# Performance work log

Measured on AMD Instinct MI355X. Metric: run time of the kernel, lower is better.

## Reference

```python
import jax, jax.numpy as jnp
import numpy as np

DIM = 128
N_HEADS = 16
HEAD_DIM = DIM // N_HEADS  # 8
HIDDEN = 344  # multiple_of=8 rounding of int(2*4*128/3)
B, S = 4, 2048


def setup_inputs() -> dict:
    key = jax.random.key(0)
    ks = jax.random.split(key, 8)
    sc = 0.05
    return {
        "x": jax.random.normal(ks[0], (B, S, DIM), dtype=jnp.float32),
        "wq": jax.random.normal(ks[1], (DIM, DIM), dtype=jnp.float32) * sc,
        "wk": jax.random.normal(ks[2], (DIM, DIM), dtype=jnp.float32) * sc,
        "wv": jax.random.normal(ks[3], (DIM, DIM), dtype=jnp.float32) * sc,
        "wo": jax.random.normal(ks[4], (DIM, DIM), dtype=jnp.float32) * sc,
        "w1": jax.random.normal(ks[5], (DIM, HIDDEN), dtype=jnp.float32) * sc,
        "w3": jax.random.normal(ks[6], (DIM, HIDDEN), dtype=jnp.float32) * sc,
        "w2": jax.random.normal(ks[7], (HIDDEN, DIM), dtype=jnp.float32) * sc,
    }


def reference(x, wq, wk, wv, wo, w1, w3, w2):
    bsz, seqlen, _ = x.shape
    # --- Attention (no scaling, no mask, per source) ---
    q = (x @ wq).reshape(bsz, seqlen, N_HEADS, HEAD_DIM)
    k = (x @ wk).reshape(bsz, seqlen, N_HEADS, HEAD_DIM)
    v = (x @ wv).reshape(bsz, seqlen, N_HEADS, HEAD_DIM)
    # scores: [B, H, S, S]
    scores = jnp.einsum("bqhd,bkhd->bhqk", q, k)
    probs = jax.nn.softmax(scores.astype(jnp.float32), axis=-1).astype(q.dtype)
    attn = jnp.einsum("bhqk,bkhd->bqhd", probs, v).reshape(bsz, seqlen, DIM)
    h = x + attn @ wo
    # --- SwiGLU FFN ---
    ffn = (jax.nn.silu(h @ w1) * (h @ w3)) @ w2
    return h + ffn
```

## Files before the change

kernel.cpp:

```cpp
#include <hip/hip_runtime.h>
#include <hip/hip_bf16.h>
#include <stdint.h>
#include <math.h>

typedef __attribute__((ext_vector_type(8))) short short8;
typedef __attribute__((ext_vector_type(4))) float f32x4;

#define NTHREADS 256
#define DIM 128
#define NH 16
#define HD 8
#define HIDDEN 344
#define HIDP 352
#define BATCH 4
#define SEQ 2048
#define MROWS (BATCH * SEQ)
#define LOG2E 1.4426950408889634f

static __device__ __forceinline__ uint16_t f2bf(float f) {
  union { float f; uint32_t u; } v; v.f = f;
  uint32_t r = v.u + 0x7FFFu + ((v.u >> 16) & 1u);
  return (uint16_t)(r >> 16);
}
static __device__ __forceinline__ uint32_t pk2(float lo, float hi) {
  union { __hip_bfloat162 b; uint32_t u; } c;
  c.b = __float22bfloat162_rn(make_float2(lo, hi));
  return c.u;
}
#define MAGIC_BF 12599163.0f
static __device__ __forceinline__ uint32_t pke2(float a, float b) {
  const float ua = fmaf(a, 128.0f, MAGIC_BF);
  const float ub = fmaf(b, 128.0f, MAGIC_BF);
  return __builtin_amdgcn_perm(__builtin_bit_cast(uint32_t, ub),
                               __builtin_bit_cast(uint32_t, ua), 0x05040100u);
}
static __device__ __forceinline__ f32x4 mfma32(short8 a, short8 b, f32x4 c) {
  return __builtin_amdgcn_mfma_f32_16x16x32_bf16(a, b, c, 0, 0, 0);
}

__global__ __launch_bounds__(256) void prep_kernel(
    const float* __restrict__ wq,
    const float* __restrict__ wk, const float* __restrict__ wv,
    const float* __restrict__ wo, const float* __restrict__ w1,
    const float* __restrict__ w3, const float* __restrict__ w2,
    uint16_t* __restrict__ qkv_t,
    uint16_t* __restrict__ wo_t,  uint16_t* __restrict__ w1_t,
    uint16_t* __restrict__ w3_t,  uint16_t* __restrict__ w2_t)
{
  const int nt  = gridDim.x * blockDim.x;
  const int tid = blockIdx.x * blockDim.x + threadIdx.x;
  for (int i = tid; i < 384 * 128; i += nt) {
    int n = i >> 7, k = i & 127;
    const float* w = (n < 128) ? wq : ((n < 256) ? wk : wv);
    const float s = (n < 128) ? LOG2E : 1.0f;
    qkv_t[i] = f2bf(w[k * 128 + (n & 127)] * s);
  }
  for (int i = tid; i < 128 * 128; i += nt) {
    int n = i >> 7, k = i & 127;
    wo_t[i] = f2bf(wo[k * 128 + n]);
  }
  for (int i = tid; i < 384 * 128; i += nt) {
    int n = i >> 7, k = i & 127;
    w1_t[i] = (n < HIDDEN) ? f2bf(w1[k * HIDDEN + n]) : (uint16_t)0;
    w3_t[i] = (n < HIDDEN) ? f2bf(w3[k * HIDDEN + n]) : (uint16_t)0;
  }
  for (int i = tid; i < 128 * HIDP; i += nt) {
    int n = i / HIDP, k = i - n * HIDP;
    w2_t[i] = (k < HIDDEN) ? f2bf(w2[k * 128 + n]) : (uint16_t)0;
  }
}

__global__ __launch_bounds__(256, 4) void qkv_gemm(
    const float* __restrict__ Av, const uint16_t* __restrict__ B1t,
    uint16_t* __restrict__ outb,
    uint16_t* __restrict__ kc_o, uint16_t* __restrict__ vt_o)
{
  const int tid = threadIdx.x;
  const int w = tid >> 6, l = tid & 63;
  const int lg = l >> 4, lm = l & 15;
  const int row0 = blockIdx.x * 64 + w * 16;
  const int col0 = blockIdx.y * 64;

  const uint16_t* Bp = B1t + (size_t)(col0 + lm) * 128 + lg * 8;
  short8 bA0 = *(const short8*)(Bp);
  short8 bA1 = *(const short8*)(Bp + 32);
  short8 bA2 = *(const short8*)(Bp + 64);
  short8 bA3 = *(const short8*)(Bp + 96);

  short8 af[4];
  const float* Af = Av + (size_t)(row0 + lm) * 128 + lg * 8;
#pragma unroll
  for (int ks = 0; ks < 4; ++ks) {
    const f32x4 a0 = *(const f32x4*)(Af + ks * 32);
    const f32x4 a1 = *(const f32x4*)(Af + ks * 32 + 4);
    union { uint32_t u[4]; short8 s8; } cv;
    cv.u[0] = pk2(a0[0], a0[1]); cv.u[1] = pk2(a0[2], a0[3]);
    cv.u[2] = pk2(a1[0], a1[1]); cv.u[3] = pk2(a1[2], a1[3]);
    af[ks] = cv.s8;
  }

  f32x4 acc[4];
#pragma unroll
  for (int t = 0; t < 4; ++t) acc[t] = (f32x4){0.f, 0.f, 0.f, 0.f};

  short8 bB0 = *(const short8*)(Bp + 2048);
  short8 bB1 = *(const short8*)(Bp + 2048 + 32);
  short8 bB2 = *(const short8*)(Bp + 2048 + 64);
  short8 bB3 = *(const short8*)(Bp + 2048 + 96);
  acc[0] = mfma32(af[0], bA0, acc[0]);
  acc[0] = mfma32(af[1], bA1, acc[0]);
  acc[0] = mfma32(af[2], bA2, acc[0]);
  acc[0] = mfma32(af[3], bA3, acc[0]);
  bA0 = *(const short8*)(Bp + 4096);
  bA1 = *(const short8*)(Bp + 4096 + 32);
  bA2 = *(const short8*)(Bp + 4096 + 64);
  bA3 = *(const short8*)(Bp + 4096 + 96);
  acc[1] = mfma32(af[0], bB0, acc[1]);
  acc[1] = mfma32(af[1], bB1, acc[1]);
  acc[1] = mfma32(af[2], bB2, acc[1]);
  acc[1] = mfma32(af[3], bB3, acc[1]);
  bB0 = *(const short8*)(Bp + 6144);
  bB1 = *(const short8*)(Bp + 6144 + 32);
  bB2 = *(const short8*)(Bp + 6144 + 64);
  bB3 = *(const short8*)(Bp + 6144 + 96);
  acc[2] = mfma32(af[0], bA0, acc[2]);
  acc[2] = mfma32(af[1], bA1, acc[2]);
  acc[2] = mfma32(af[2], bA2, acc[2]);
  acc[2] = mfma32(af[3], bA3, acc[2]);
  acc[3] = mfma32(af[0], bB0, acc[3]);
  acc[3] = mfma32(af[1], bB1, acc[3]);
  acc[3] = mfma32(af[2], bB2, acc[3]);
  acc[3] = mfma32(af[3], bB3, acc[3]);

#pragma unroll
  for (int t = 0; t < 4; ++t) {
#pragma unroll
    for (int r = 0; r < 4; ++r) {
      const int row = row0 + lg * 4 + r;
      const int col = col0 + t * 16 + lm;
      const float v = acc[t][r];
      const int bb = row >> 11, ss = row & 2047;
      if (col < 128) {
        outb[(size_t)row * 128 + col] = f2bf(v);
      } else if (col < 256) {
        const int c = col - 128;
        kc_o[((size_t)((bb << 4) + (c >> 3)) * SEQ + ss) * 8 + (c & 7)] = f2bf(v);
      } else {
        const int c = col - 256;
        vt_o[((size_t)(bb * 128 + c)) * SEQ + ss] = f2bf(v);
      }
    }
  }
}

__global__ __launch_bounds__(256, 4) void attn_kernel(
    const uint16_t* __restrict__ qb,
    const uint16_t* __restrict__ kc,
    const uint16_t* __restrict__ vt,
    uint16_t* __restrict__ attn_o)
{
  __shared__ __attribute__((aligned(16))) float part[4][64][32];

  const int tid = threadIdx.x;
  const int w = tid >> 6, l = tid & 63;
  const int lg = l >> 4, lm = l & 15;
  int bid = blockIdx.x;
  bid = (bid & 7) * 128 + (bid >> 3);
  const int qc = bid & 15;
  const int bh = bid >> 4;
  const int b = bh >> 4, h = bh & 15;
  const int q0 = qc * 128;
  const int kh = w;

  const short8 zero8 = {0, 0, 0, 0, 0, 0, 0, 0};
  const f32x4 zero4 = {0.f, 0.f, 0.f, 0.f};
  const short ob = (short)0x3F80;
  const short8 ones8 = {ob, ob, ob, ob, ob, ob, ob, ob};

  short8 qf[8];
#pragma unroll
  for (int t = 0; t < 8; ++t) {
    qf[t] = zero8;
    if (lg == 0)
      qf[t] = *(const short8*)(qb + (size_t)(b * SEQ + q0 + t * 16 + lm) * DIM + h * HD);
  }

  const uint16_t* kp = kc + (size_t)bh * SEQ * HD +
                       (kh * 512 + 8 * (lm >> 2) + (lm & 3)) * HD;
  const uint16_t* vp = vt + (size_t)(bh * HD + (lm & 7)) * SEQ + kh * 512 + lg * 8;

  short8 k0 = zero8, k1 = zero8, k2 = zero8, k3 = zero8;
  short8 v0 = (lm == 8) ? ones8 : zero8;
  short8 v1 = v0;

  f32x4 acc[8];
#pragma unroll
  for (int t = 0; t < 8; ++t) acc[t] = zero4;

#define LK()                                       \
  do { if (lg == 0) {                              \
    k0 = *(const short8*)(kp);                     \
    k1 = *(const short8*)(kp + 32);                \
    k2 = *(const short8*)(kp + 256);               \
    k3 = *(const short8*)(kp + 288); }             \
    kp += 512; } while (0)

#define LV()                                       \
  do { if (lm < HD) {                              \
    v0 = *(const short8*)(vp);                     \
    v1 = *(const short8*)(vp + 32); }              \
    vp += 64; } while (0)

#define PACKP(SA, SB, OUT)                 \
  do { union { uint32_t u[4]; short8 s; } _t; \
    _t.u[0] = pke2(SA[0], SA[1]);          \
    _t.u[1] = pke2(SA[2], SA[3]);          \
    _t.u[2] = pke2(SB[0], SB[1]);          \
    _t.u[3] = pke2(SB[2], SB[3]);          \
    OUT = _t.s; } while (0)

  LK();
  LV();

#pragma unroll 1
  for (int it = 0; it < 8; ++it) {
#pragma unroll
    for (int t = 0; t < 8; ++t) {
      f32x4 s0 = mfma32(k0, qf[t], zero4);
      f32x4 s1 = mfma32(k1, qf[t], zero4);
      f32x4 s2 = mfma32(k2, qf[t], zero4);
      f32x4 s3 = mfma32(k3, qf[t], zero4);
      if (t == 7) LK();
      short8 p0, p1;
      PACKP(s0, s1, p0);
      PACKP(s2, s3, p1);
      acc[t] = mfma32(v0, p0, acc[t]);
      acc[t] = mfma32(v1, p1, acc[t]);
      if (t == 7) LV();
    }
  }

#undef LK
#undef LV
#undef PACKP

#pragma unroll
  for (int t = 0; t < 8; ++t) *(f32x4*)&part[w][l][t * 4] = acc[t];
  __syncthreads();

#pragma unroll
  for (int j = 0; j < 2; ++j) {
    const int tt = w * 2 + j;
    const f32x4 m = (*(const f32x4*)&part[0][l][tt * 4] +
                     *(const f32x4*)&part[1][l][tt * 4]) +
                    (*(const f32x4*)&part[2][l][tt * 4] +
                     *(const f32x4*)&part[3][l][tt * 4]);
    const float inv = 1.0f / __shfl(m[0], 32 + lm);
    if (lg < 2) {
      const size_t o = (size_t)(b * SEQ + q0 + tt * 16 + lm) * DIM + h * HD + lg * 4;
      *(uint32_t*)(attn_o + o)     = pk2(m[0] * inv, m[1] * inv);
      *(uint32_t*)(attn_o + o + 2) = pk2(m[2] * inv, m[3] * inv);
    }
  }
}

__global__ __launch_bounds__(512, 4) void ffn_kernel(
    const uint16_t* __restrict__ attn_o,
    const float* __restrict__ x,
    const uint16_t* __restrict__ wo_t,
    const uint16_t* __restrict__ w1_t,
    const uint16_t* __restrict__ w3_t,
    const uint16_t* __restrict__ w2_t,
    float* __restrict__ out)
{
  __shared__ __attribute__((aligned(16))) uint16_t h_l[16][136];
  __shared__ __attribute__((aligned(16))) uint16_t u_l[16][360];

  const int tid = threadIdx.x;
  const int w = tid >> 6, l = tid & 63;
  const int lg = l >> 4, lm = l & 15;
  const int R0 = blockIdx.x * 16;

  short8 af[4], wof[4], b1a[4], b3a[4];
  {
    const uint16_t* Ap = attn_o + (size_t)(R0 + lm) * 128 + lg * 8;
    const uint16_t* Bp = wo_t + (size_t)(w * 16 + lm) * 128 + lg * 8;
    const uint16_t* B1p = w1_t + (size_t)(w * 16 + lm) * 128 + lg * 8;
    const uint16_t* B3p = w3_t + (size_t)(w * 16 + lm) * 128 + lg * 8;
#pragma unroll
    for (int ks = 0; ks < 4; ++ks) {
      af[ks]  = *(const short8*)(Ap + ks * 32);
      wof[ks] = *(const short8*)(Bp + ks * 32);
      b1a[ks] = *(const short8*)(B1p + ks * 32);
      b3a[ks] = *(const short8*)(B3p + ks * 32);
    }
  }

  float hreg[4];
  {
    f32x4 a0 = (f32x4){0.f, 0.f, 0.f, 0.f};
    f32x4 a1 = (f32x4){0.f, 0.f, 0.f, 0.f};
    a0 = mfma32(af[0], wof[0], a0);
    a1 = mfma32(af[1], wof[1], a1);
    a0 = mfma32(af[2], wof[2], a0);
    a1 = mfma32(af[3], wof[3], a1);
    const f32x4 acc = a0 + a1;
#pragma unroll
    for (int r = 0; r < 4; ++r) {
      const float h = acc[r] + x[(size_t)(R0 + lg * 4 + r) * 128 + w * 16 + lm];
      hreg[r] = h;
      h_l[lg * 4 + r][w * 16 + lm] = f2bf(h);
    }
  }
  __syncthreads();

  short8 af2[4];
#pragma unroll
  for (int ks = 0; ks < 4; ++ks)
    af2[ks] = *(const short8*)&h_l[lm][ks * 32 + lg * 8];

  {
    f32x4 ag = (f32x4){0.f, 0.f, 0.f, 0.f};
    f32x4 ae = (f32x4){0.f, 0.f, 0.f, 0.f};
#pragma unroll
    for (int ks = 0; ks < 4; ++ks) {
      ag = mfma32(af2[ks], b1a[ks], ag);
      ae = mfma32(af2[ks], b3a[ks], ae);
    }
    const int ct2 = w + 8;
    const uint16_t* B1p = w1_t + (size_t)(ct2 * 16 + lm) * 128 + lg * 8;
    const uint16_t* B3p = w3_t + (size_t)(ct2 * 16 + lm) * 128 + lg * 8;
#pragma unroll
    for (int ks = 0; ks < 4; ++ks) {
      b1a[ks] = *(const short8*)(B1p + ks * 32);
      b3a[ks] = *(const short8*)(B3p + ks * 32);
    }
#pragma unroll
    for (int r = 0; r < 4; ++r) {
      const float g = ag[r];
      const float u = g / (1.f + __expf(-g)) * ae[r];
      u_l[lg * 4 + r][w * 16 + lm] = f2bf(u);
    }
  }
  {
    const int ct = w + 8;
    f32x4 ag = (f32x4){0.f, 0.f, 0.f, 0.f};
    f32x4 ae = (f32x4){0.f, 0.f, 0.f, 0.f};
#pragma unroll
    for (int ks = 0; ks < 4; ++ks) {
      ag = mfma32(af2[ks], b1a[ks], ag);
      ae = mfma32(af2[ks], b3a[ks], ae);
    }
    if (w < 6) {
      const int ct3 = w + 16;
      const uint16_t* B1p = w1_t + (size_t)(ct3 * 16 + lm) * 128 + lg * 8;
      const uint16_t* B3p = w3_t + (size_t)(ct3 * 16 + lm) * 128 + lg * 8;
#pragma unroll
      for (int ks = 0; ks < 4; ++ks) {
        b1a[ks] = *(const short8*)(B1p + ks * 32);
        b3a[ks] = *(const short8*)(B3p + ks * 32);
      }
    }
#pragma unroll
    for (int r = 0; r < 4; ++r) {
      const float g = ag[r];
      const float u = g / (1.f + __expf(-g)) * ae[r];
      u_l[lg * 4 + r][ct * 16 + lm] = f2bf(u);
    }
  }
  if (w < 6) {
    const int ct = w + 16;
    f32x4 ag = (f32x4){0.f, 0.f, 0.f, 0.f};
    f32x4 ae = (f32x4){0.f, 0.f, 0.f, 0.f};
#pragma unroll
    for (int ks = 0; ks < 4; ++ks) {
      ag = mfma32(af2[ks], b1a[ks], ag);
      ae = mfma32(af2[ks], b3a[ks], ae);
    }
#pragma unroll
    for (int r = 0; r < 4; ++r) {
      const float g = ag[r];
      const float u = g / (1.f + __expf(-g)) * ae[r];
      u_l[lg * 4 + r][ct * 16 + lm] = f2bf(u);
    }
  }
  __syncthreads();

  {
    short8 w2f0, w2f1, w2f2, w2f3;
    const uint16_t* Bp = w2_t + (size_t)(w * 16 + lm) * HIDP + lg * 8;
    w2f0 = *(const short8*)(Bp);
    w2f1 = *(const short8*)(Bp + 32);
    w2f2 = *(const short8*)(Bp + 64);
    w2f3 = *(const short8*)(Bp + 96);
    f32x4 acce = (f32x4){0.f, 0.f, 0.f, 0.f};
    f32x4 acco = (f32x4){0.f, 0.f, 0.f, 0.f};
    acce = mfma32(*(const short8*)&u_l[lm][0 * 32 + lg * 8], w2f0, acce);
    w2f0 = *(const short8*)(Bp + 128);
    acco = mfma32(*(const short8*)&u_l[lm][1 * 32 + lg * 8], w2f1, acco);
    w2f1 = *(const short8*)(Bp + 160);
    acce = mfma32(*(const short8*)&u_l[lm][2 * 32 + lg * 8], w2f2, acce);
    w2f2 = *(const short8*)(Bp + 192);
    acco = mfma32(*(const short8*)&u_l[lm][3 * 32 + lg * 8], w2f3, acco);
    w2f3 = *(const short8*)(Bp + 224);
    acce = mfma32(*(const short8*)&u_l[lm][4 * 32 + lg * 8], w2f0, acce);
    w2f0 = *(const short8*)(Bp + 256);
    acco = mfma32(*(const short8*)&u_l[lm][5 * 32 + lg * 8], w2f1, acco);
    w2f1 = *(const short8*)(Bp + 288);
    acce = mfma32(*(const short8*)&u_l[lm][6 * 32 + lg * 8], w2f2, acce);
    w2f2 = *(const short8*)(Bp + 320);
    acco = mfma32(*(const short8*)&u_l[lm][7 * 32 + lg * 8], w2f3, acco);
    acce = mfma32(*(const short8*)&u_l[lm][8 * 32 + lg * 8], w2f0, acce);
    acco = mfma32(*(const short8*)&u_l[lm][9 * 32 + lg * 8], w2f1, acco);
    acce = mfma32(*(const short8*)&u_l[lm][10 * 32 + lg * 8], w2f2, acce);
    const f32x4 acc = acce + acco;
#pragma unroll
    for (int r = 0; r < 4; ++r)
      out[(size_t)(R0 + lg * 4 + r) * 128 + w * 16 + lm] = hreg[r] + acc[r];
  }
}

extern "C" void kernel_launch(void* const* d_in, const int* in_sizes, int n_in,
                              void* d_out, int out_size, void* d_ws, size_t ws_size,
                              hipStream_t stream) {
  const float* x  = (const float*)d_in[0];
  const float* wq = (const float*)d_in[1];
  const float* wk = (const float*)d_in[2];
  const float* wv = (const float*)d_in[3];
  const float* wo = (const float*)d_in[4];
  const float* w1 = (const float*)d_in[5];
  const float* w3 = (const float*)d_in[6];
  const float* w2 = (const float*)d_in[7];
  float* out = (float*)d_out;

  char* ws = (char*)d_ws;
  size_t off = 0;
  auto alloc = [&](size_t bytes) {
    size_t o = off;
    off += (bytes + 255) & ~(size_t)255;
    return o;
  };
  uint16_t* qkv_t  = (uint16_t*)(ws + alloc(384 * 128 * 2));
  uint16_t* wo_t   = (uint16_t*)(ws + alloc(128 * 128 * 2));
  uint16_t* w1_t   = (uint16_t*)(ws + alloc(384 * 128 * 2));
  uint16_t* w3_t   = (uint16_t*)(ws + alloc(384 * 128 * 2));
  uint16_t* w2_t   = (uint16_t*)(ws + alloc(128 * HIDP * 2));
  uint16_t* q_buf  = (uint16_t*)(ws + alloc((size_t)MROWS * DIM * 2));
  uint16_t* kc_b   = (uint16_t*)(ws + alloc((size_t)MROWS * DIM * 2));
  uint16_t* vt_b   = (uint16_t*)(ws + alloc((size_t)MROWS * DIM * 2));
  uint16_t* attn_o = (uint16_t*)(ws + alloc((size_t)MROWS * DIM * 2));

  prep_kernel<<<512, 256, 0, stream>>>(wq, wk, wv, wo, w1, w3, w2,
                                       qkv_t, wo_t, w1_t, w3_t, w2_t);
  qkv_gemm<<<dim3(MROWS / 64, 6), 256, 0, stream>>>(
      x, qkv_t, q_buf, kc_b, vt_b);
  attn_kernel<<<dim3(BATCH * NH * (SEQ / 128)), 256, 0, stream>>>(
      q_buf, kc_b, vt_b, attn_o);
  ffn_kernel<<<dim3(MROWS / 16), 512, 0, stream>>>(
      attn_o, x, wo_t, w1_t, w3_t, w2_t, out);
}
```

Baseline: 63.52 us.

## Process 32 rows per FFN block to reuse weight fragments across two row tiles

The FFN kernel now handles two 16-row tiles per block, so each loaded wo/w1/w3/w2 weight fragment feeds two MFMAs instead of one. This halves the per-row weight fragment traffic from L2 and doubles the independent MFMA chains. The grid is halved, and register and LDS use per block grow, so the launch bound drops to 2 blocks per CU, which reduces occupancy.

```diff
diff --git a/kernel.cpp b/kernel.cpp
--- a/kernel.cpp
+++ b/kernel.cpp
@@ -264,7 +264,7 @@
   }
 }
 
-__global__ __launch_bounds__(512, 4) void ffn_kernel(
+__global__ __launch_bounds__(512, 2) void ffn_kernel(
     const uint16_t* __restrict__ attn_o,
     const float* __restrict__ x,
     const uint16_t* __restrict__ wo_t,
@@ -273,117 +273,104 @@
     const uint16_t* __restrict__ w2_t,
     float* __restrict__ out)
 {
-  __shared__ __attribute__((aligned(16))) uint16_t h_l[16][136];
-  __shared__ __attribute__((aligned(16))) uint16_t u_l[16][360];
+  __shared__ __attribute__((aligned(16))) uint16_t h_l[2][16][136];
+  __shared__ __attribute__((aligned(16))) uint16_t u_l[2][16][360];
 
   const int tid = threadIdx.x;
   const int w = tid >> 6, l = tid & 63;
   const int lg = l >> 4, lm = l & 15;
-  const int R0 = blockIdx.x * 16;
-
-  short8 af[4], wof[4], b1a[4], b3a[4];
+  const int R0 = blockIdx.x * 32;
+
+  short8 af0[4], af1[4], wof[4], b1a[4], b3a[4];
   {
-    const uint16_t* Ap = attn_o + (size_t)(R0 + lm) * 128 + lg * 8;
+    const uint16_t* Ap0 = attn_o + (size_t)(R0 + lm) * 128 + lg * 8;
+    const uint16_t* Ap1 = attn_o + (size_t)(R0 + 16 + lm) * 128 + lg * 8;
     const uint16_t* Bp = wo_t + (size_t)(w * 16 + lm) * 128 + lg * 8;
     const uint16_t* B1p = w1_t + (size_t)(w * 16 + lm) * 128 + lg * 8;
     const uint16_t* B3p = w3_t + (size_t)(w * 16 + lm) * 128 + lg * 8;
 #pragma unroll
     for (int ks = 0; ks < 4; ++ks) {
-      af[ks]  = *(const short8*)(Ap + ks * 32);
+      af0[ks] = *(const short8*)(Ap0 + ks * 32);
+      af1[ks] = *(const short8*)(Ap1 + ks * 32);
       wof[ks] = *(const short8*)(Bp + ks * 32);
       b1a[ks] = *(const short8*)(B1p + ks * 32);
       b3a[ks] = *(const short8*)(B3p + ks * 32);
     }
   }
 
-  float hreg[4];
+  float h0reg[4], h1reg[4];
   {
-    f32x4 a0 = (f32x4){0.f, 0.f, 0.f, 0.f};
-    f32x4 a1 = (f32x4){0.f, 0.f, 0.f, 0.f};
-    a0 = mfma32(af[0], wof[0], a0);
-    a1 = mfma32(af[1], wof[1], a1);
-    a0 = mfma32(af[2], wof[2], a0);
-    a1 = mfma32(af[3], wof[3], a1);
-    const f32x4 acc = a0 + a1;
+    f32x4 p00 = (f32x4){0.f, 0.f, 0.f, 0.f};
+    f32x4 p01 = (f32x4){0.f, 0.f, 0.f, 0.f};
+    f32x4 p10 = (f32x4){0.f, 0.f, 0.f, 0.f};
+    f32x4 p11 = (f32x4){0.f, 0.f, 0.f, 0.f};
+    p00 = mfma32(af0[0], wof[0], p00);
+    p10 = mfma32(af1[0], wof[0], p10);
+    p01 = mfma32(af0[1], wof[1], p01);
+    p11 = mfma32(af1[1], wof[1], p11);
+    p00 = mfma32(af0[2], wof[2], p00);
+    p10 = mfma32(af1[2], wof[2], p10);
+    p01 = mfma32(af0[3], wof[3], p01);
+    p11 = mfma32(af1[3], wof[3], p11);
+    const f32x4 a0 = p00 + p01;
+    const f32x4 a1 = p10 + p11;
 #pragma unroll
     for (int r = 0; r < 4; ++r) {
-      const float h = acc[r] + x[(size_t)(R0 + lg * 4 + r) * 128 + w * 16 + lm];
-      hreg[r] = h;
-      h_l[lg * 4 + r][w * 16 + lm] = f2bf(h);
+      const float h0 = a0[r] + x[(size_t)(R0 + lg * 4 + r) * 128 + w * 16 + lm];
+      const float h1 = a1[r] + x[(size_t)(R0 + 16 + lg * 4 + r) * 128 + w * 16 + lm];
+      h0reg[r] = h0;
+      h1reg[r] = h1;
+      h_l[0][lg * 4 + r][w * 16 + lm] = f2bf(h0);
+      h_l[1][lg * 4 + r][w * 16 + lm] = f2bf(h1);
     }
   }
   __syncthreads();
 
-  short8 af2[4];
-#pragma unroll
-  for (int ks = 0; ks < 4; ++ks)
-    af2[ks] = *(const short8*)&h_l[lm][ks * 32 + lg * 8];
-
-  {
-    f32x4 ag = (f32x4){0.f, 0.f, 0.f, 0.f};
-    f32x4 ae = (f32x4){0.f, 0.f, 0.f, 0.f};
-#pragma unroll
-    for (int ks = 0; ks < 4; ++ks) {
-      ag = mfma32(af2[ks], b1a[ks], ag);
-      ae = mfma32(af2[ks], b3a[ks], ae);
-    }
-    const int ct2 = w + 8;
-    const uint16_t* B1p = w1_t + (size_t)(ct2 * 16 + lm) * 128 + lg * 8;
-    const uint16_t* B3p = w3_t + (size_t)(ct2 * 16 + lm) * 128 + lg * 8;
-#pragma unroll
-    for (int ks = 0; ks < 4; ++ks) {
-      b1a[ks] = *(const short8*)(B1p + ks * 32);
-      b3a[ks] = *(const short8*)(B3p + ks * 32);
-    }
-#pragma unroll
-    for (int r = 0; r < 4; ++r) {
-      const float g = ag[r];
-      const float u = g / (1.f + __expf(-g)) * ae[r];
-      u_l[lg * 4 + r][w * 16 + lm] = f2bf(u);
-    }
-  }
-  {
-    const int ct = w + 8;
-    f32x4 ag = (f32x4){0.f, 0.f, 0.f, 0.f};
-    f32x4 ae = (f32x4){0.f, 0.f, 0.f, 0.f};
-#pragma unroll
-    for (int ks = 0; ks < 4; ++ks) {
-      ag = mfma32(af2[ks], b1a[ks], ag);
-      ae = mfma32(af2[ks], b3a[ks], ae);
-    }
-    if (w < 6) {
-      const int ct3 = w + 16;
-      const uint16_t* B1p = w1_t + (size_t)(ct3 * 16 + lm) * 128 + lg * 8;
-      const uint16_t* B3p = w3_t + (size_t)(ct3 * 16 + lm) * 128 + lg * 8;
-#pragma unroll
-      for (int ks = 0; ks < 4; ++ks) {
-        b1a[ks] = *(const short8*)(B1p + ks * 32);
-        b3a[ks] = *(const short8*)(B3p + ks * 32);
-      }
-    }
-#pragma unroll
-    for (int r = 0; r < 4; ++r) {
-      const float g = ag[r];
-      const float u = g / (1.f + __expf(-g)) * ae[r];
-      u_l[lg * 4 + r][ct * 16 + lm] = f2bf(u);
-    }
-  }
-  if (w < 6) {
-    const int ct = w + 16;
-    f32x4 ag = (f32x4){0.f, 0.f, 0.f, 0.f};
-    f32x4 ae = (f32x4){0.f, 0.f, 0.f, 0.f};
-#pragma unroll
-    for (int ks = 0; ks < 4; ++ks) {
-      ag = mfma32(af2[ks], b1a[ks], ag);
-      ae = mfma32(af2[ks], b3a[ks], ae);
-    }
-#pragma unroll
-    for (int r = 0; r < 4; ++r) {
-      const float g = ag[r];
-      const float u = g / (1.f + __expf(-g)) * ae[r];
-      u_l[lg * 4 + r][ct * 16 + lm] = f2bf(u);
-    }
-  }
+  short8 afh0[4], afh1[4];
+#pragma unroll
+  for (int ks = 0; ks < 4; ++ks) {
+    afh0[ks] = *(const short8*)&h_l[0][lm][ks * 32 + lg * 8];
+    afh1[ks] = *(const short8*)&h_l[1][lm][ks * 32 + lg * 8];
+  }
+
+#define BSTAGE(CT, PREFETCH_CT, DO_PREFETCH)                        \
+  do {                                                              \
+    f32x4 g0 = (f32x4){0.f, 0.f, 0.f, 0.f};                         \
+    f32x4 e0 = (f32x4){0.f, 0.f, 0.f, 0.f};                         \
+    f32x4 g1 = (f32x4){0.f, 0.f, 0.f, 0.f};                         \
+    f32x4 e1 = (f32x4){0.f, 0.f, 0.f, 0.f};                         \
+    _Pragma("unroll")                                               \
+    for (int ks = 0; ks < 4; ++ks) {                                \
+      g0 = mfma32(afh0[ks], b1a[ks], g0);                           \
+      g1 = mfma32(afh1[ks], b1a[ks], g1);                           \
+      e0 = mfma32(afh0[ks], b3a[ks], e0);                           \
+      e1 = mfma32(afh1[ks], b3a[ks], e1);                           \
+    }                                                               \
+    if (DO_PREFETCH) {                                              \
+      const uint16_t* B1p = w1_t + (size_t)((PREFETCH_CT) * 16 + lm) * 128 + lg * 8; \
+      const uint16_t* B3p = w3_t + (size_t)((PREFETCH_CT) * 16 + lm) * 128 + lg * 8; \
+      _Pragma("unroll")                                             \
+      for (int ks = 0; ks < 4; ++ks) {                              \
+        b1a[ks] = *(const short8*)(B1p + ks * 32);                  \
+        b3a[ks] = *(const short8*)(B3p + ks * 32);                  \
+      }                                                             \
+    }                                                               \
+    _Pragma("unroll")                                               \
+    for (int r = 0; r < 4; ++r) {                                   \
+      const float ga = g0[r];                                       \
+      const float gb = g1[r];                                       \
+      const float u0 = ga / (1.f + __expf(-ga)) * e0[r];            \
+      const float u1 = gb / (1.f + __expf(-gb)) * e1[r];            \
+      u_l[0][lg * 4 + r][(CT) * 16 + lm] = f2bf(u0);                \
+      u_l[1][lg * 4 + r][(CT) * 16 + lm] = f2bf(u1);                \
+    }                                                               \
+  } while (0)
+
+  BSTAGE(w, w + 8, 1);
+  BSTAGE(w + 8, w + 16, (w < 6));
+  if (w < 6) BSTAGE(w + 16, 0, 0);
+
+#undef BSTAGE
   __syncthreads();
 
   {
@@ -393,30 +380,33 @@
     w2f1 = *(const short8*)(Bp + 32);
     w2f2 = *(const short8*)(Bp + 64);
     w2f3 = *(const short8*)(Bp + 96);
-    f32x4 acce = (f32x4){0.f, 0.f, 0.f, 0.f};
-    f32x4 acco = (f32x4){0.f, 0.f, 0.f, 0.f};
-    acce = mfma32(*(const short8*)&u_l[lm][0 * 32 + lg * 8], w2f0, acce);
-    w2f0 = *(const short8*)(Bp + 128);
-    acco = mfma32(*(const short8*)&u_l[lm][1 * 32 + lg * 8], w2f1, acco);
-    w2f1 = *(const short8*)(Bp + 160);
-    acce = mfma32(*(const short8*)&u_l[lm][2 * 32 + lg * 8], w2f2, acce);
-    w2f2 = *(const short8*)(Bp + 192);
-    acco = mfma32(*(const short8*)&u_l[lm][3 * 32 + lg * 8], w2f3, acco);
-    w2f3 = *(const short8*)(Bp + 224);
-    acce = mfma32(*(const short8*)&u_l[lm][4 * 32 + lg * 8], w2f0, acce);
-    w2f0 = *(const short8*)(Bp + 256);
-    acco = mfma32(*(const short8*)&u_l[lm][5 * 32 + lg * 8], w2f1, acco);
-    w2f1 = *(const short8*)(Bp + 288);
-    acce = mfma32(*(const short8*)&u_l[lm][6 * 32 + lg * 8], w2f2, acce);
-    w2f2 = *(const short8*)(Bp + 320);
-    acco = mfma32(*(const short8*)&u_l[lm][7 * 32 + lg * 8], w2f3, acco);
-    acce = mfma32(*(const short8*)&u_l[lm][8 * 32 + lg * 8], w2f0, acce);
-    acco = mfma32(*(const short8*)&u_l[lm][9 * 32 + lg * 8], w2f1, acco);
-    acce = mfma32(*(const short8*)&u_l[lm][10 * 32 + lg * 8], w2f2, acce);
-    const f32x4 acc = acce + acco;
-#pragma unroll
-    for (int r = 0; r < 4; ++r)
-      out[(size_t)(R0 + lg * 4 + r) * 128 + w * 16 + lm] = hreg[r] + acc[r];
+    f32x4 c0 = (f32x4){0.f, 0.f, 0.f, 0.f};
+    f32x4 c1 = (f32x4){0.f, 0.f, 0.f, 0.f};
+#define CSTEP(K2, WF, RELOAD_OFF, DO_RELOAD)                        \
+    do {                                                            \
+      const short8 u0 = *(const short8*)&u_l[0][lm][(K2) * 32 + lg * 8]; \
+      const short8 u1 = *(const short8*)&u_l[1][lm][(K2) * 32 + lg * 8]; \
+      c0 = mfma32(u0, WF, c0);                                      \
+      c1 = mfma32(u1, WF, c1);                                      \
+      if (DO_RELOAD) WF = *(const short8*)(Bp + (RELOAD_OFF));      \
+    } while (0)
+    CSTEP(0, w2f0, 128, 1);
+    CSTEP(1, w2f1, 160, 1);
+    CSTEP(2, w2f2, 192, 1);
+    CSTEP(3, w2f3, 224, 1);
+    CSTEP(4, w2f0, 256, 1);
+    CSTEP(5, w2f1, 288, 1);
+    CSTEP(6, w2f2, 320, 1);
+    CSTEP(7, w2f3, 0, 0);
+    CSTEP(8, w2f0, 0, 0);
+    CSTEP(9, w2f1, 0, 0);
+    CSTEP(10, w2f2, 0, 0);
+#undef CSTEP
+#pragma unroll
+    for (int r = 0; r < 4; ++r) {
+      out[(size_t)(R0 + lg * 4 + r) * 128 + w * 16 + lm] = h0reg[r] + c0[r];
+      out[(size_t)(R0 + 16 + lg * 4 + r) * 128 + w * 16 + lm] = h1reg[r] + c1[r];
+    }
   }
 }
 
@@ -456,6 +446,6 @@
       x, qkv_t, q_buf, kc_b, vt_b);
   attn_kernel<<<dim3(BATCH * NH * (SEQ / 128)), 256, 0, stream>>>(
       q_buf, kc_b, vt_b, attn_o);
-  ffn_kernel<<<dim3(MROWS / 16), 512, 0, stream>>>(
+  ffn_kernel<<<dim3(MROWS / 32), 512, 0, stream>>>(
       attn_o, x, wo_t, w1_t, w3_t, w2_t, out);
 }
```

Result: faster. 57.16 us, median of 3 (-10.0%).
